# Optimization experiments

Hardware: AMD Instinct MI355X
Metric: run time of the kernel (lower is better)

Reference implementation:

```python
import jax, jax.numpy as jnp
import numpy as np

N = 524288
MAXV = 8  # rect-rect intersection has at most 8 vertices
EPS = 1e-8


def setup_inputs() -> dict:
    key = jax.random.key(0)
    k1, k2, k3 = jax.random.split(key, 3)
    return {
        "box": jax.random.normal(k1, (N, 11), jnp.float32),
        "box_target": jax.random.normal(k2, (N, 11), jnp.float32),
        "weight": jax.random.uniform(k3, (N, 11), jnp.float32),
        "avg_factor": N // 2,
    }


def decode_box(box):
    # [x,y,z,logW,logL,logH,sin,cos,v...] -> [x,y,z,W,L,H,yaw,v...]
    yaw = jnp.arctan2(box[..., 6], box[..., 7])
    return jnp.concatenate(
        [box[..., :3], jnp.exp(box[..., 3:6]), yaw[..., None], box[..., 8:]], axis=-1)


def get_rect_vertices(bev):
    # bev: (5,) = [cx, cy, w, l, yaw] -> (4, 2) corners, CCW, rotated about center
    cx, cy, w, l, yaw = bev[0], bev[1], bev[2], bev[3], bev[4]
    dx, dy = w / 2, l / 2
    lx = jnp.stack([-dx, dx, dx, -dx])
    ly = jnp.stack([-dy, -dy, dy, dy])
    s, c = jnp.sin(yaw), jnp.cos(yaw)
    return jnp.stack([lx * c - ly * s + cx, lx * s + ly * c + cy], axis=-1)


def clip_halfplane(poly, count, a, b):
    # Sutherland-Hodgman clip of poly (MAXV,2) with `count` valid verts
    # against left side of directed edge a->b. Fixed-size buffer + mask.
    d = b - a  # (2,)
    idx = jnp.arange(MAXV)
    cnt = jnp.maximum(count, 1)
    prev = poly[(idx - 1) % cnt]
    cur = poly

    def is_left(p):
        return d[0] * (p[..., 1] - a[1]) - d[1] * (p[..., 0] - a[0]) >= 0

    cur_in, prev_in = is_left(cur), is_left(prev)
    num = (a[0] - prev[:, 0]) * d[1] - (a[1] - prev[:, 1]) * d[0]
    den = (cur[:, 0] - prev[:, 0]) * d[1] - (cur[:, 1] - prev[:, 1]) * d[0] + EPS
    ip = prev + (num / den)[:, None] * (cur - prev)  # edge/halfplane intersection
    valid = idx < count
    emit_ip = valid & (prev_in ^ cur_in)   # crossing edge -> emit intersection
    emit_cur = valid & cur_in              # inside vertex -> emit it
    # interleave per-input-edge outputs in original order (ip, then cur)
    pts = jnp.stack([ip, cur], axis=1).reshape(2 * MAXV, 2)
    emit = jnp.stack([emit_ip, emit_cur], axis=1).reshape(2 * MAXV)
    pos = jnp.where(emit, jnp.cumsum(emit) - 1, MAXV)  # compact valid pts to front
    out = jnp.zeros((MAXV, 2), poly.dtype).at[pos].set(
        jnp.where(emit[:, None], pts, 0.0), mode="drop")
    return out, jnp.minimum(emit.sum(), MAXV).astype(jnp.int32)


def poly_area(poly, count):
    # shoelace over the `count` valid vertices
    idx = jnp.arange(MAXV)
    nxt = poly[(idx + 1) % jnp.maximum(count, 1)]
    cross = jnp.where(idx < count, poly[:, 0] * nxt[:, 1] - poly[:, 1] * nxt[:, 0], 0.0)
    return jnp.abs(cross.sum() / 2.0)


def giou_one(bev1, bev2):
    v1 = get_rect_vertices(bev1)  # (4,2)
    v2 = get_rect_vertices(bev2)
    poly = jnp.zeros((MAXV, 2), bev1.dtype).at[:4].set(v1)
    count = jnp.int32(4)
    for i in range(4):  # clip subject rect by 4 half-planes of clip rect
        poly, count = clip_halfplane(poly, count, v2[i], v2[(i + 1) % 4])
        count = jnp.where(count < 3, 0, count)  # degenerate -> empty (original break)
    inter = poly_area(poly, count)
    area1 = bev1[2] * bev1[3]
    area2 = bev2[2] * bev2[3]
    union = area1 + area2 - inter
    allp = jnp.concatenate([v1, v2], axis=0)
    enclosing = (allp[:, 0].max() - allp[:, 0].min()) * (allp[:, 1].max() - allp[:, 1].min())
    iou = inter / (union + EPS)
    return iou - (enclosing - union) / (enclosing + EPS)


def _bev(dec):
    return jnp.stack([dec[:, 0], dec[:, 1], dec[:, 3], dec[:, 4], dec[:, 6]], axis=-1)


def reference(box, box_target, weight, avg_factor):
    af = max(float(avg_factor), 1.0)
    # L1 box loss (reg_weights are all 1.0 per init defaults)
    loss_box = (jnp.abs(box - box_target) * weight).sum() / af
    # rotated BEV GIoU loss
    bev_p = _bev(decode_box(box))
    bev_t = _bev(decode_box(box_target))
    giou = jax.vmap(giou_one)(bev_p, bev_t)
    loss_giou = (1.0 - giou).sum() / af
    return loss_box, loss_giou
```

## Files before the change

### kernel.cpp

```cpp
#include <hip/hip_runtime.h>

#define BLOCK 256
#define ITERS 4
#define EPSF 1e-8f

typedef float f4u __attribute__((ext_vector_type(4), aligned(4)));

struct Row9 { f4u b0, b1, b2, t0, t1, t2, w0, w1, w2; };

__device__ __forceinline__ Row9 load_row(const float* __restrict__ box,
                                         const float* __restrict__ tgt,
                                         const float* __restrict__ wgt,
                                         size_t r) {
    Row9 R;
    R.b0 = *(const f4u*)(box + r); R.b1 = *(const f4u*)(box + r + 4); R.b2 = *(const f4u*)(box + r + 7);
    R.t0 = *(const f4u*)(tgt + r); R.t1 = *(const f4u*)(tgt + r + 4); R.t2 = *(const f4u*)(tgt + r + 7);
    R.w0 = *(const f4u*)(wgt + r); R.w1 = *(const f4u*)(wgt + r + 4); R.w2 = *(const f4u*)(wgt + r + 7);
    return R;
}

__device__ __forceinline__ float safe_rcp(float d) {
    float sd = (fabsf(d) > 1e-30f) ? d : copysignf(1e-30f, d);
    return __frcp_rn(sd);
}

__device__ __forceinline__ float clip_len(float px, float py,
                                          float rdx, float rdy,
                                          float hx, float hy) {
    float t1x = (-hx - px) * rdx, t2x = (hx - px) * rdx;
    float t1y = (-hy - py) * rdy, t2y = (hy - py) * rdy;
    float tmin = fmaxf(fmaxf(fminf(t1x, t2x), fminf(t1y, t2y)), 0.f);
    float tmax = fminf(fminf(fmaxf(t1x, t2x), fmaxf(t1y, t2y)), 1.f);
    return fmaxf(tmax - tmin, 0.f);
}

__device__ __forceinline__ void box_compute(const Row9& R, float& l1out, float& gout)
{
    f4u b0 = R.b0, b1 = R.b1, b2 = R.b2;
    f4u t0 = R.t0, t1 = R.t1, t2 = R.t2;
    f4u w0 = R.w0, w1 = R.w1, w2 = R.w2;

    float lb = 0.f;
    lb += fabsf(b0.x - t0.x) * w0.x;
    lb += fabsf(b0.y - t0.y) * w0.y;
    lb += fabsf(b0.z - t0.z) * w0.z;
    lb += fabsf(b0.w - t0.w) * w0.w;
    lb += fabsf(b1.x - t1.x) * w1.x;
    lb += fabsf(b1.y - t1.y) * w1.y;
    lb += fabsf(b1.z - t1.z) * w1.z;
    lb += fabsf(b1.w - t1.w) * w1.w;
    lb += fabsf(b2.y - t2.y) * w2.y;
    lb += fabsf(b2.z - t2.z) * w2.z;
    lb += fabsf(b2.w - t2.w) * w2.w;
    l1out = lb;

    float cx1 = b0.x, cy1 = b0.y, cx2 = t0.x, cy2 = t0.y;
    float w1v = __expf(b0.w), l1v = __expf(b1.x);
    float w2v = __expf(t0.w), l2v = __expf(t1.x);
    float r1 = rsqrtf(fmaxf(b1.z * b1.z + b1.w * b1.w, 1e-30f));
    float s1 = b1.z * r1, c1 = b1.w * r1;
    float r2 = rsqrtf(fmaxf(t1.z * t1.z + t1.w * t1.w, 1e-30f));
    float s2 = t1.z * r2, c2 = t1.w * r2;

    float hx1 = 0.5f * w1v, hy1 = 0.5f * l1v;
    float hx2 = 0.5f * w2v, hy2 = 0.5f * l2v;

    float e1x = fabsf(hx1 * c1) + fabsf(hy1 * s1);
    float e1y = fabsf(hx1 * s1) + fabsf(hy1 * c1);
    float e2x = fabsf(hx2 * c2) + fabsf(hy2 * s2);
    float e2y = fabsf(hx2 * s2) + fabsf(hy2 * c2);
    float enc = (fmaxf(cx1 + e1x, cx2 + e2x) - fminf(cx1 - e1x, cx2 - e2x))
              * (fmaxf(cy1 + e1y, cy2 + e2y) - fminf(cy1 - e1y, cy2 - e2y));

    float dxw = cx1 - cx2, dyw = cy1 - cy2;
    float txl =  c2 * dxw + s2 * dyw;
    float tyl = -s2 * dxw + c2 * dyw;
    float cr_ = c1 * c2 + s1 * s2;
    float sr_ = s1 * c2 - c1 * s2;

    float ax_ = hx1 * cr_, ay_ = hx1 * sr_;
    float bx_ = hy1 * sr_, by_ = hy1 * cr_;
    float q0x = txl - ax_ + bx_, q0y = tyl - ay_ - by_;
    float q1x = txl + ax_ + bx_, q1y = tyl + ay_ - by_;
    float q2x = txl + ax_ - bx_, q2y = tyl + ay_ + by_;
    float q3x = txl - ax_ - bx_, q3y = tyl - ay_ + by_;

    float inter2 = 0.f;

    {
        float d01x = 2.f * ax_, d01y = 2.f * ay_;
        float d12x = -2.f * bx_, d12y = 2.f * by_;
        float r01x = safe_rcp(d01x), r01y = safe_rcp(d01y);
        float r12x = safe_rcp(d12x), r12y = safe_rcp(d12y);

        float L0 = clip_len(q0x, q0y,  r01x,  r01y, hx2, hy2);
        inter2 += L0 * (q0x * d01y - q0y * d01x);
        float L1 = clip_len(q1x, q1y,  r12x,  r12y, hx2, hy2);
        inter2 += L1 * (q1x * d12y - q1y * d12x);
        float L2 = clip_len(q2x, q2y, -r01x, -r01y, hx2, hy2);
        inter2 += L2 * (q2y * d01x - q2x * d01y);
        float L3 = clip_len(q3x, q3y, -r12x, -r12y, hx2, hy2);
        inter2 += L3 * (q3y * d12x - q3x * d12y);
    }

    {
        float zx = -hx2 - txl, zy = -hy2 - tyl;
        float u0x =  cr_ * zx + sr_ * zy;
        float u0y = -sr_ * zx + cr_ * zy;
        float E0x =  2.f * hx2 * cr_, E0y = -2.f * hx2 * sr_;
        float E1x =  2.f * hy2 * sr_, E1y =  2.f * hy2 * cr_;
        float u1x = u0x + E0x, u1y = u0y + E0y;
        float u2x = u1x + E1x, u2y = u1y + E1y;
        float u3x = u0x + E1x, u3y = u0y + E1y;
        float re0x = safe_rcp(E0x), re0y = safe_rcp(E0y);
        float re1x = safe_rcp(E1x), re1y = safe_rcp(E1y);

        float tsum = 0.f;
        tsum += clip_len(u0x, u0y,  re0x,  re0y, hx1, hy1);
        tsum += clip_len(u1x, u1y,  re1x,  re1y, hx1, hy1);
        tsum += clip_len(u2x, u2y, -re0x, -re0y, hx1, hy1);
        tsum += clip_len(u3x, u3y, -re1x, -re1y, hx1, hy1);
        inter2 += 2.f * hx2 * hy2 * tsum;
    }

    float inter = 0.5f * fabsf(inter2);
    float areaU = w1v * l1v + w2v * l2v - inter;
    float iou = inter / (areaU + EPSF);
    float giou = iou - (enc - areaU) / (enc + EPSF);
    gout = 1.f - giou;
}

__global__ __launch_bounds__(BLOCK) void box_loss_main(
    const float* __restrict__ box, const float* __restrict__ tgt,
    const float* __restrict__ wgt, int n, int T, float* __restrict__ partials)
{
    __shared__ float red[8];

    const int tid = threadIdx.x;
    int i = blockIdx.x * BLOCK + tid;
    float sumL1 = 0.f, sumG = 0.f;

    bool v = i < n;
    Row9 cur = load_row(box, tgt, wgt, (size_t)(v ? i : 0) * 11);

#pragma unroll
    for (int k = 0; k < ITERS; ++k) {
        int inext = i + T;
        bool vnext = false;
        Row9 nxt;
        if (k + 1 < ITERS) {
            vnext = inext < n;
            nxt = load_row(box, tgt, wgt, (size_t)(vnext ? inext : 0) * 11);
        }
        float l1, g;
        box_compute(cur, l1, g);
        sumL1 += v ? l1 : 0.f;
        sumG  += v ? g  : 0.f;
        if (k + 1 < ITERS) { cur = nxt; v = vnext; i = inext; }
    }

#pragma unroll
    for (int off = 32; off > 0; off >>= 1) {
        sumL1 += __shfl_down(sumL1, off);
        sumG  += __shfl_down(sumG, off);
    }
    const int wave = tid >> 6, lane = tid & 63;
    if (lane == 0) { red[wave] = sumL1; red[4 + wave] = sumG; }
    __syncthreads();
    if (tid == 0) {
        partials[2 * (size_t)blockIdx.x]     = red[0] + red[1] + red[2] + red[3];
        partials[2 * (size_t)blockIdx.x + 1] = red[4] + red[5] + red[6] + red[7];
    }
}

__global__ __launch_bounds__(256) void box_loss_final(
    const float* __restrict__ partials, int nblk,
    const int* __restrict__ avg_factor, float* __restrict__ out)
{
    __shared__ float red[8];
    float a = 0.f, g = 0.f;
    for (int i = threadIdx.x; i < nblk; i += 256) {
        a += partials[2 * (size_t)i];
        g += partials[2 * (size_t)i + 1];
    }
#pragma unroll
    for (int off = 32; off > 0; off >>= 1) {
        a += __shfl_down(a, off);
        g += __shfl_down(g, off);
    }
    const int wave = threadIdx.x >> 6, lane = threadIdx.x & 63;
    if (lane == 0) { red[wave] = a; red[4 + wave] = g; }
    __syncthreads();
    if (threadIdx.x == 0) {
        float af = (float)(*avg_factor);
        if (af < 1.f) af = 1.f;
        out[0] = (red[0] + red[1] + red[2] + red[3]) / af;
        out[1] = (red[4] + red[5] + red[6] + red[7]) / af;
    }
}

extern "C" void kernel_launch(void* const* d_in, const int* in_sizes, int n_in,
                              void* d_out, int out_size, void* d_ws, size_t ws_size,
                              hipStream_t stream) {
    const float* box = (const float*)d_in[0];
    const float* tgt = (const float*)d_in[1];
    const float* wgt = (const float*)d_in[2];
    const int*   af  = (const int*)d_in[3];
    float* out = (float*)d_out;
    float* partials = (float*)d_ws;

    int n = in_sizes[0] / 11;
    int nblk = (n + BLOCK * ITERS - 1) / (BLOCK * ITERS);
    if (nblk < 1) nblk = 1;
    int T = nblk * BLOCK;

    hipLaunchKernelGGL(box_loss_main, dim3(nblk), dim3(BLOCK), 0, stream,
                       box, tgt, wgt, n, T, partials);
    hipLaunchKernelGGL(box_loss_final, dim3(1), dim3(256), 0, stream,
                       partials, nblk, af, out);
}
```

Baseline: 19.63 us.

## Process two rows per thread with packed float2 math, doubling grid

```diff
diff --git a/kernel.cpp b/kernel.cpp
--- a/kernel.cpp
+++ b/kernel.cpp
@@ -1,17 +1,18 @@
 #include <hip/hip_runtime.h>
 
 #define BLOCK 256
-#define ITERS 4
 #define EPSF 1e-8f
 
 typedef float f4u __attribute__((ext_vector_type(4), aligned(4)));
+typedef float pf2 __attribute__((ext_vector_type(2)));
 
 struct Row9 { f4u b0, b1, b2, t0, t1, t2, w0, w1, w2; };
 
 __device__ __forceinline__ Row9 load_row(const float* __restrict__ box,
                                          const float* __restrict__ tgt,
                                          const float* __restrict__ wgt,
-                                         size_t r) {
+                                         int row) {
+    const size_t r = (size_t)row * 11;
     Row9 R;
     R.b0 = *(const f4u*)(box + r); R.b1 = *(const f4u*)(box + r + 4); R.b2 = *(const f4u*)(box + r + 7);
     R.t0 = *(const f4u*)(tgt + r); R.t1 = *(const f4u*)(tgt + r + 4); R.t2 = *(const f4u*)(tgt + r + 7);
@@ -19,115 +20,119 @@
     return R;
 }
 
-__device__ __forceinline__ float safe_rcp(float d) {
+__device__ __forceinline__ pf2 mk(float a, float b) { pf2 r; r.x = a; r.y = b; return r; }
+__device__ __forceinline__ pf2 sp(float v) { pf2 r; r.x = v; r.y = v; return r; }
+__device__ __forceinline__ pf2 pmin(pf2 a, pf2 b) { return __builtin_elementwise_min(a, b); }
+__device__ __forceinline__ pf2 pmax(pf2 a, pf2 b) { return __builtin_elementwise_max(a, b); }
+__device__ __forceinline__ pf2 pabs(pf2 a) { return __builtin_elementwise_abs(a); }
+
+__device__ __forceinline__ float srcp1(float d) {
     float sd = (fabsf(d) > 1e-30f) ? d : copysignf(1e-30f, d);
     return __frcp_rn(sd);
 }
-
-__device__ __forceinline__ float clip_len(float px, float py,
-                                          float rdx, float rdy,
-                                          float hx, float hy) {
-    float t1x = (-hx - px) * rdx, t2x = (hx - px) * rdx;
-    float t1y = (-hy - py) * rdy, t2y = (hy - py) * rdy;
-    float tmin = fmaxf(fmaxf(fminf(t1x, t2x), fminf(t1y, t2y)), 0.f);
-    float tmax = fminf(fminf(fmaxf(t1x, t2x), fmaxf(t1y, t2y)), 1.f);
-    return fmaxf(tmax - tmin, 0.f);
-}
-
-__device__ __forceinline__ void box_compute(const Row9& R, float& l1out, float& gout)
+__device__ __forceinline__ pf2 srcp(pf2 d) { pf2 r; r.x = srcp1(d.x); r.y = srcp1(d.y); return r; }
+__device__ __forceinline__ pf2 pexp(pf2 d) { pf2 r; r.x = __expf(d.x); r.y = __expf(d.y); return r; }
+__device__ __forceinline__ pf2 prsq(pf2 d) { pf2 r; r.x = rsqrtf(d.x); r.y = rsqrtf(d.y); return r; }
+__device__ __forceinline__ pf2 prcp(pf2 d) { pf2 r; r.x = __frcp_rn(d.x); r.y = __frcp_rn(d.y); return r; }
+
+__device__ __forceinline__ pf2 clip_len2(pf2 px, pf2 py, pf2 rdx, pf2 rdy,
+                                         pf2 hx, pf2 hy) {
+    pf2 t1x = (-hx - px) * rdx, t2x = (hx - px) * rdx;
+    pf2 t1y = (-hy - py) * rdy, t2y = (hy - py) * rdy;
+    pf2 tmin = pmax(pmax(pmin(t1x, t2x), pmin(t1y, t2y)), sp(0.f));
+    pf2 tmax = pmin(pmin(pmax(t1x, t2x), pmax(t1y, t2y)), sp(1.f));
+    return pmax(tmax - tmin, sp(0.f));
+}
+
+#define PK(m) mk(A.m, B.m)
+
+__device__ __forceinline__ void pair_compute(const Row9& A, const Row9& B,
+                                             pf2& l1out, pf2& gout)
 {
-    f4u b0 = R.b0, b1 = R.b1, b2 = R.b2;
-    f4u t0 = R.t0, t1 = R.t1, t2 = R.t2;
-    f4u w0 = R.w0, w1 = R.w1, w2 = R.w2;
-
-    float lb = 0.f;
-    lb += fabsf(b0.x - t0.x) * w0.x;
-    lb += fabsf(b0.y - t0.y) * w0.y;
-    lb += fabsf(b0.z - t0.z) * w0.z;
-    lb += fabsf(b0.w - t0.w) * w0.w;
-    lb += fabsf(b1.x - t1.x) * w1.x;
-    lb += fabsf(b1.y - t1.y) * w1.y;
-    lb += fabsf(b1.z - t1.z) * w1.z;
-    lb += fabsf(b1.w - t1.w) * w1.w;
-    lb += fabsf(b2.y - t2.y) * w2.y;
-    lb += fabsf(b2.z - t2.z) * w2.z;
-    lb += fabsf(b2.w - t2.w) * w2.w;
+    pf2 lb;
+    lb  = pabs(PK(b0.x) - PK(t0.x)) * PK(w0.x);
+    lb += pabs(PK(b0.y) - PK(t0.y)) * PK(w0.y);
+    lb += pabs(PK(b0.z) - PK(t0.z)) * PK(w0.z);
+    lb += pabs(PK(b0.w) - PK(t0.w)) * PK(w0.w);
+    lb += pabs(PK(b1.x) - PK(t1.x)) * PK(w1.x);
+    lb += pabs(PK(b1.y) - PK(t1.y)) * PK(w1.y);
+    lb += pabs(PK(b1.z) - PK(t1.z)) * PK(w1.z);
+    lb += pabs(PK(b1.w) - PK(t1.w)) * PK(w1.w);
+    lb += pabs(PK(b2.y) - PK(t2.y)) * PK(w2.y);
+    lb += pabs(PK(b2.z) - PK(t2.z)) * PK(w2.z);
+    lb += pabs(PK(b2.w) - PK(t2.w)) * PK(w2.w);
     l1out = lb;
 
-    float cx1 = b0.x, cy1 = b0.y, cx2 = t0.x, cy2 = t0.y;
-    float w1v = __expf(b0.w), l1v = __expf(b1.x);
-    float w2v = __expf(t0.w), l2v = __expf(t1.x);
-    float r1 = rsqrtf(fmaxf(b1.z * b1.z + b1.w * b1.w, 1e-30f));
-    float s1 = b1.z * r1, c1 = b1.w * r1;
-    float r2 = rsqrtf(fmaxf(t1.z * t1.z + t1.w * t1.w, 1e-30f));
-    float s2 = t1.z * r2, c2 = t1.w * r2;
-
-    float hx1 = 0.5f * w1v, hy1 = 0.5f * l1v;
-    float hx2 = 0.5f * w2v, hy2 = 0.5f * l2v;
-
-    float e1x = fabsf(hx1 * c1) + fabsf(hy1 * s1);
-    float e1y = fabsf(hx1 * s1) + fabsf(hy1 * c1);
-    float e2x = fabsf(hx2 * c2) + fabsf(hy2 * s2);
-    float e2y = fabsf(hx2 * s2) + fabsf(hy2 * c2);
-    float enc = (fmaxf(cx1 + e1x, cx2 + e2x) - fminf(cx1 - e1x, cx2 - e2x))
-              * (fmaxf(cy1 + e1y, cy2 + e2y) - fminf(cy1 - e1y, cy2 - e2y));
-
-    float dxw = cx1 - cx2, dyw = cy1 - cy2;
-    float txl =  c2 * dxw + s2 * dyw;
-    float tyl = -s2 * dxw + c2 * dyw;
-    float cr_ = c1 * c2 + s1 * s2;
-    float sr_ = s1 * c2 - c1 * s2;
-
-    float ax_ = hx1 * cr_, ay_ = hx1 * sr_;
-    float bx_ = hy1 * sr_, by_ = hy1 * cr_;
-    float q0x = txl - ax_ + bx_, q0y = tyl - ay_ - by_;
-    float q1x = txl + ax_ + bx_, q1y = tyl + ay_ - by_;
-    float q2x = txl + ax_ - bx_, q2y = tyl + ay_ + by_;
-    float q3x = txl - ax_ - bx_, q3y = tyl - ay_ + by_;
-
-    float inter2 = 0.f;
-
+    pf2 cx1 = PK(b0.x), cy1 = PK(b0.y), cx2 = PK(t0.x), cy2 = PK(t0.y);
+    pf2 w1v = pexp(PK(b0.w)), l1v = pexp(PK(b1.x));
+    pf2 w2v = pexp(PK(t0.w)), l2v = pexp(PK(t1.x));
+    pf2 sy1 = PK(b1.z), cw1 = PK(b1.w), sy2 = PK(t1.z), cw2 = PK(t1.w);
+    pf2 r1 = prsq(pmax(sy1 * sy1 + cw1 * cw1, sp(1e-30f)));
+    pf2 s1 = sy1 * r1, c1 = cw1 * r1;
+    pf2 r2 = prsq(pmax(sy2 * sy2 + cw2 * cw2, sp(1e-30f)));
+    pf2 s2 = sy2 * r2, c2 = cw2 * r2;
+
+    pf2 hx1 = 0.5f * w1v, hy1 = 0.5f * l1v;
+    pf2 hx2 = 0.5f * w2v, hy2 = 0.5f * l2v;
+
+    pf2 e1x = pabs(hx1 * c1) + pabs(hy1 * s1);
+    pf2 e1y = pabs(hx1 * s1) + pabs(hy1 * c1);
+    pf2 e2x = pabs(hx2 * c2) + pabs(hy2 * s2);
+    pf2 e2y = pabs(hx2 * s2) + pabs(hy2 * c2);
+    pf2 enc = (pmax(cx1 + e1x, cx2 + e2x) - pmin(cx1 - e1x, cx2 - e2x))
+            * (pmax(cy1 + e1y, cy2 + e2y) - pmin(cy1 - e1y, cy2 - e2y));
+
+    pf2 dxw = cx1 - cx2, dyw = cy1 - cy2;
+    pf2 txl =  c2 * dxw + s2 * dyw;
+    pf2 tyl = -s2 * dxw + c2 * dyw;
+    pf2 cr = c1 * c2 + s1 * s2;
+    pf2 sr = s1 * c2 - c1 * s2;
+
+    pf2 ax = hx1 * cr, ay = hx1 * sr;
+    pf2 bx = hy1 * sr, by = hy1 * cr;
+    pf2 q0x = txl - ax + bx, q0y = tyl - ay - by;
+    pf2 q1x = txl + ax + bx, q1y = tyl + ay - by;
+    pf2 q2x = txl + ax - bx, q2y = tyl + ay + by;
+    pf2 q3x = txl - ax - bx, q3y = tyl - ay + by;
+
+    pf2 inter2 = sp(0.f);
     {
-        float d01x = 2.f * ax_, d01y = 2.f * ay_;
-        float d12x = -2.f * bx_, d12y = 2.f * by_;
-        float r01x = safe_rcp(d01x), r01y = safe_rcp(d01y);
-        float r12x = safe_rcp(d12x), r12y = safe_rcp(d12y);
-
-        float L0 = clip_len(q0x, q0y,  r01x,  r01y, hx2, hy2);
+        pf2 d01x = 2.f * ax, d01y = 2.f * ay;
+        pf2 d12x = -2.f * bx, d12y = 2.f * by;
+        pf2 r01x = srcp(d01x), r01y = srcp(d01y);
+        pf2 r12x = srcp(d12x), r12y = srcp(d12y);
+        pf2 L0 = clip_len2(q0x, q0y, r01x, r01y, hx2, hy2);
         inter2 += L0 * (q0x * d01y - q0y * d01x);
-        float L1 = clip_len(q1x, q1y,  r12x,  r12y, hx2, hy2);
+        pf2 L1 = clip_len2(q1x, q1y, r12x, r12y, hx2, hy2);
         inter2 += L1 * (q1x * d12y - q1y * d12x);
-        float L2 = clip_len(q2x, q2y, -r01x, -r01y, hx2, hy2);
+        pf2 L2 = clip_len2(q2x, q2y, -r01x, -r01y, hx2, hy2);
         inter2 += L2 * (q2y * d01x - q2x * d01y);
-        float L3 = clip_len(q3x, q3y, -r12x, -r12y, hx2, hy2);
+        pf2 L3 = clip_len2(q3x, q3y, -r12x, -r12y, hx2, hy2);
         inter2 += L3 * (q3y * d12x - q3x * d12y);
     }
-
     {
-        float zx = -hx2 - txl, zy = -hy2 - tyl;
-        float u0x =  cr_ * zx + sr_ * zy;
-        float u0y = -sr_ * zx + cr_ * zy;
-        float E0x =  2.f * hx2 * cr_, E0y = -2.f * hx2 * sr_;
-        float E1x =  2.f * hy2 * sr_, E1y =  2.f * hy2 * cr_;
-        float u1x = u0x + E0x, u1y = u0y + E0y;
-        float u2x = u1x + E1x, u2y = u1y + E1y;
-        float u3x = u0x + E1x, u3y = u0y + E1y;
-        float re0x = safe_rcp(E0x), re0y = safe_rcp(E0y);
-        float re1x = safe_rcp(E1x), re1y = safe_rcp(E1y);
-
-        float tsum = 0.f;
-        tsum += clip_len(u0x, u0y,  re0x,  re0y, hx1, hy1);
-        tsum += clip_len(u1x, u1y,  re1x,  re1y, hx1, hy1);
-        tsum += clip_len(u2x, u2y, -re0x, -re0y, hx1, hy1);
-        tsum += clip_len(u3x, u3y, -re1x, -re1y, hx1, hy1);
-        inter2 += 2.f * hx2 * hy2 * tsum;
-    }
-
-    float inter = 0.5f * fabsf(inter2);
-    float areaU = w1v * l1v + w2v * l2v - inter;
-    float iou = inter / (areaU + EPSF);
-    float giou = iou - (enc - areaU) / (enc + EPSF);
-    gout = 1.f - giou;
+        pf2 zx = -hx2 - txl, zy = -hy2 - tyl;
+        pf2 u0x =  cr * zx + sr * zy;
+        pf2 u0y = -sr * zx + cr * zy;
+        pf2 E0x =  2.f * hx2 * cr, E0y = -2.f * hx2 * sr;
+        pf2 E1x =  2.f * hy2 * sr, E1y =  2.f * hy2 * cr;
+        pf2 u1x = u0x + E0x, u1y = u0y + E0y;
+        pf2 u2x = u1x + E1x, u2y = u1y + E1y;
+        pf2 u3x = u0x + E1x, u3y = u0y + E1y;
+        pf2 re0x = srcp(E0x), re0y = srcp(E0y);
+        pf2 re1x = srcp(E1x), re1y = srcp(E1y);
+        pf2 tsum = clip_len2(u0x, u0y, re0x, re0y, hx1, hy1);
+        tsum += clip_len2(u1x, u1y, re1x, re1y, hx1, hy1);
+        tsum += clip_len2(u2x, u2y, -re0x, -re0y, hx1, hy1);
+        tsum += clip_len2(u3x, u3y, -re1x, -re1y, hx1, hy1);
+        inter2 += 2.f * (hx2 * hy2) * tsum;
+    }
+
+    pf2 inter = 0.5f * pabs(inter2);
+    pf2 areaU = w1v * l1v + w2v * l2v - inter;
+    pf2 iou = inter * prcp(areaU + sp(EPSF));
+    pf2 giou = iou - (enc - areaU) * prcp(enc + sp(EPSF));
+    gout = sp(1.f) - giou;
 }
 
 __global__ __launch_bounds__(BLOCK) void box_loss_main(
@@ -137,27 +142,18 @@
     __shared__ float red[8];
 
     const int tid = threadIdx.x;
-    int i = blockIdx.x * BLOCK + tid;
-    float sumL1 = 0.f, sumG = 0.f;
-
-    bool v = i < n;
-    Row9 cur = load_row(box, tgt, wgt, (size_t)(v ? i : 0) * 11);
-
-#pragma unroll
-    for (int k = 0; k < ITERS; ++k) {
-        int inext = i + T;
-        bool vnext = false;
-        Row9 nxt;
-        if (k + 1 < ITERS) {
-            vnext = inext < n;
-            nxt = load_row(box, tgt, wgt, (size_t)(vnext ? inext : 0) * 11);
-        }
-        float l1, g;
-        box_compute(cur, l1, g);
-        sumL1 += v ? l1 : 0.f;
-        sumG  += v ? g  : 0.f;
-        if (k + 1 < ITERS) { cur = nxt; v = vnext; i = inext; }
-    }
+    const int iA = blockIdx.x * BLOCK + tid;
+    const int iB = iA + T;
+    const bool hasA = iA < n, hasB = iB < n;
+
+    Row9 A = load_row(box, tgt, wgt, hasA ? iA : 0);
+    Row9 B = load_row(box, tgt, wgt, hasB ? iB : 0);
+
+    pf2 l1, g;
+    pair_compute(A, B, l1, g);
+
+    float sumL1 = (hasA ? l1.x : 0.f) + (hasB ? l1.y : 0.f);
+    float sumG  = (hasA ? g.x  : 0.f) + (hasB ? g.y  : 0.f);
 
 #pragma unroll
     for (int off = 32; off > 0; off >>= 1) {
@@ -210,7 +206,7 @@
     float* partials = (float*)d_ws;
 
     int n = in_sizes[0] / 11;
-    int nblk = (n + BLOCK * ITERS - 1) / (BLOCK * ITERS);
+    int nblk = (n + BLOCK * 2 - 1) / (BLOCK * 2);
     if (nblk < 1) nblk = 1;
     int T = nblk * BLOCK;
 
```

After: 20.28 us. 1.03x slower.
